# Performance work log

Hardware: AMD Instinct MI355X
Metric: run time of the kernel (lower is better)

## Reference

```python
import jax, jax.numpy as jnp
import numpy as np

B, T, N_EMBD = 4, 2048, 1024
NUM_EXPERTS, TOP_K = 8, 2
N_CITIES = 4
LIN = N_EMBD + 32 + N_EMBD // 4 + N_EMBD // 4 + N_EMBD // 8 + N_EMBD // 8  # 1824


def setup_inputs() -> dict:
    key = jax.random.key(0)
    ks = jax.random.split(key, 12)
    s = 0.02  # init std as in _init_weights
    return {
        "x": jax.random.normal(ks[0], (B, T, N_EMBD), jnp.float32),
        "delta_t_info": jax.random.normal(ks[1], (B, T, N_EMBD // 4), jnp.float32),
        "delta_dis_info": jax.random.normal(ks[2], (B, T, N_EMBD // 4), jnp.float32),
        "delta_rg_info": jax.random.normal(ks[3], (B, T, N_EMBD // 8), jnp.float32),
        "delta_entropy_info": jax.random.normal(ks[4], (B, T, N_EMBD // 8), jnp.float32),
        "city_embeddings": jax.random.normal(ks[5], (N_CITIES, 32), jnp.float32),
        "Wg": jax.random.normal(ks[6], (LIN, NUM_EXPERTS), jnp.float32) * s,
        "bg": jnp.zeros((NUM_EXPERTS,), jnp.float32),
        "W1": jax.random.normal(ks[7], (NUM_EXPERTS, N_EMBD, 4 * N_EMBD), jnp.float32) * s,
        "b1": jnp.zeros((NUM_EXPERTS, 4 * N_EMBD), jnp.float32),
        "W2": jax.random.normal(ks[8], (NUM_EXPERTS, 4 * N_EMBD, N_EMBD), jnp.float32) * s,
        "b2": jnp.zeros((NUM_EXPERTS, N_EMBD), jnp.float32),
        "city_index": 1,
    }


def _moe(x, dt, dd, drg, de, city_embeddings, Wg, bg, W1, b1, W2, b2, city_index):
    b, t, _ = x.shape
    city = jnp.broadcast_to(city_embeddings[city_index], (b, t, 32))
    feats = jnp.concatenate([x, city, dt, dd, drg, de], axis=-1)  # [B,T,LIN]
    logits = jnp.einsum("btl,le->bte", feats, Wg) + bg            # eval mode: no noise
    gate1 = jax.nn.softmax(logits, axis=-1)
    _, topi = jax.lax.top_k(logits, TOP_K)                        # [B,T,k]
    # mask of top-k experts per token; scatter(-inf elsewhere) + softmax
    mask = jax.nn.one_hot(topi, NUM_EXPERTS, dtype=jnp.float32).sum(axis=-2) > 0
    sparse_logits = jnp.where(mask, logits, -jnp.inf)
    gates = jax.nn.softmax(sparse_logits, axis=-1)                # zeros outside top-k
    out = jnp.zeros_like(x)
    for e in range(NUM_EXPERTS):  # fixed small expert set
        h = jax.nn.gelu(jnp.einsum("btc,ch->bth", x, W1[e]) + b1[e], approximate=True)
        y = jnp.einsum("bth,hc->btc", h, W2[e]) + b2[e]
        out = out + gates[..., e:e + 1] * y  # gate is exactly 0 for non-topk tokens
    return out, gate1


def reference(x, delta_t_info, delta_dis_info, delta_rg_info, delta_entropy_info,
              city_embeddings, Wg, bg, W1, b1, W2, b2, city_index):
    return _moe(x, delta_t_info, delta_dis_info, delta_rg_info, delta_entropy_info,
                city_embeddings, Wg, bg, W1, b1, W2, b2, city_index)
```

## Files before the change

### kernel.cpp

```cpp
#include <hip/hip_runtime.h>
#include <hip/hip_bf16.h>
#include <stdint.h>

#define NTOK 8192
#define DEMB 1024
#define HDIM 4096
#define NEXP 8
#define LINF 1824
#define MAXPAD 17280

typedef __attribute__((ext_vector_type(8))) __bf16 bf16x8;
typedef __attribute__((ext_vector_type(4))) __bf16 bf16x4v;
typedef __attribute__((ext_vector_type(4))) float f32x4;

__device__ __forceinline__ void gload_lds16(const void* g, void* l) {
  __builtin_amdgcn_global_load_lds(
      (const __attribute__((address_space(1))) void*)g,
      (__attribute__((address_space(3))) void*)l, 16, 0, 0);
}

__device__ __forceinline__ float dot4(float4 a, float4 b) {
  return a.x*b.x + a.y*b.y + a.z*b.z + a.w*b.w;
}

__global__ void __launch_bounds__(256) k_logits(
    const float* __restrict__ x, const float* __restrict__ dt,
    const float* __restrict__ dd, const float* __restrict__ drg,
    const float* __restrict__ de, const float* __restrict__ city,
    const float* __restrict__ Wg, const float* __restrict__ bg,
    const int* __restrict__ city_index,
    float* __restrict__ gate1, int* __restrict__ top_i, float2* __restrict__ top_g)
{
  __shared__ float WgT[NEXP * LINF];
  const int tid = threadIdx.x;
  const float4* Wg4 = (const float4*)Wg;
  for (int i = tid; i < LINF * NEXP / 4; i += 256) {
    float4 v = Wg4[i];
    int e0 = (i & 1) * 4, f = i >> 1;
    WgT[(e0+0)*LINF + f] = v.x; WgT[(e0+1)*LINF + f] = v.y;
    WgT[(e0+2)*LINF + f] = v.z; WgT[(e0+3)*LINF + f] = v.w;
  }
  __syncthreads();

  const int wave = tid >> 6, lane = tid & 63;
  const int ci = city_index[0];
  const float4* city4 = (const float4*)(city + ci*32);
  const float4 z4 = {0.f, 0.f, 0.f, 0.f};

  #pragma unroll
  for (int k = 0; k < 4; ++k) {
    const int t = blockIdx.x*16 + wave*4 + k;
    const float4* x4 = (const float4*)x + (size_t)t*256;
    float4 xv0 = x4[lane], xv1 = x4[64+lane], xv2 = x4[128+lane], xv3 = x4[192+lane];
    float4 cv = (lane < 8) ? city4[lane] : z4;
    float4 tv = ((const float4*)dt)[(size_t)t*64 + lane];
    float4 dv = ((const float4*)dd)[(size_t)t*64 + lane];
    float4 rv = z4, ev = z4;
    if (lane < 32) {
      rv = ((const float4*)drg)[(size_t)t*32 + lane];
      ev = ((const float4*)de )[(size_t)t*32 + lane];
    }
    float a[8];
    const int l8 = lane & 7, l32 = lane & 31;
    #pragma unroll
    for (int e = 0; e < 8; ++e) {
      const float4* W = (const float4*)(WgT + e*LINF);
      float s = dot4(xv0, W[lane]) + dot4(xv1, W[64+lane])
              + dot4(xv2, W[128+lane]) + dot4(xv3, W[192+lane]);
      s += dot4(cv, W[256 + l8]);
      s += dot4(tv, W[264 + lane]) + dot4(dv, W[328 + lane]);
      s += dot4(rv, W[392 + l32]) + dot4(ev, W[424 + l32]);
      a[e] = s;
    }
    #pragma unroll
    for (int off = 32; off > 0; off >>= 1)
      #pragma unroll
      for (int e = 0; e < 8; ++e) a[e] += __shfl_xor(a[e], off);

    float lg[8];
    #pragma unroll
    for (int e = 0; e < 8; ++e) lg[e] = a[e] + bg[e];
    float mx = lg[0];
    #pragma unroll
    for (int e = 1; e < 8; ++e) mx = fmaxf(mx, lg[e]);
    float ex[8]; float s = 0.f;
    #pragma unroll
    for (int e = 0; e < 8; ++e) { ex[e] = expf(lg[e] - mx); s += ex[e]; }
    int i1 = 0; float l1 = lg[0];
    #pragma unroll
    for (int e = 1; e < 8; ++e) if (lg[e] > l1) { l1 = lg[e]; i1 = e; }
    int i2 = -1; float l2 = -1e30f;
    #pragma unroll
    for (int e = 0; e < 8; ++e) if (e != i1 && lg[e] > l2) { l2 = lg[e]; i2 = e; }
    float e2 = expf(l2 - l1);

    if (lane == 0) {
      float inv = 1.f / s;
      float4 o0 = { ex[0]*inv, ex[1]*inv, ex[2]*inv, ex[3]*inv };
      float4 o1 = { ex[4]*inv, ex[5]*inv, ex[6]*inv, ex[7]*inv };
      float4* gp = (float4*)(gate1 + (size_t)t*8);
      gp[0] = o0; gp[1] = o1;
      top_i[t] = i1 | (i2 << 4);
      float2 g = { 1.f / (1.f + e2), e2 / (1.f + e2) };
      top_g[t] = g;
    }
  }
}

__global__ void __launch_bounds__(256) k_build(
    const int* __restrict__ top_i, const float2* __restrict__ top_g,
    int* __restrict__ counts, int* __restrict__ ex_tok, float* __restrict__ ex_gate,
    int2* __restrict__ ppos)
{
  __shared__ int lcnt[8], lbase[8];
  const int tid = threadIdx.x;
  if (tid < 8) lcnt[tid] = 0;
  __syncthreads();
  const int t = blockIdx.x*256 + tid;
  const int ti = top_i[t];
  const int i1 = ti & 15, i2 = ti >> 4;
  const float2 g = top_g[t];
  int p1 = atomicAdd(&lcnt[i1], 1);
  int p2 = atomicAdd(&lcnt[i2], 1);
  __syncthreads();
  if (tid < 8) lbase[tid] = atomicAdd(&counts[tid], lcnt[tid]);
  __syncthreads();
  int s1 = lbase[i1] + p1; ex_tok[i1*NTOK+s1] = t; ex_gate[i1*NTOK+s1] = g.x;
  int s2 = lbase[i2] + p2; ex_tok[i2*NTOK+s2] = t; ex_gate[i2*NTOK+s2] = g.y;
  int2 pp = { i1 | (s1 << 3), i2 | (s2 << 3) };
  ppos[t] = pp;
}

__global__ void k_finalize(const int* __restrict__ counts, int* __restrict__ seg) {
  if (threadIdx.x == 0 && blockIdx.x == 0) {
    int s = 0;
    for (int e = 0; e < 8; ++e) { seg[e] = s; s += (counts[e] + 127) & ~127; }
    seg[8] = s;
  }
}

__global__ void __launch_bounds__(256) k_conv_x(
    const float4* __restrict__ x, bf16x4v* __restrict__ xb, int n4)
{
  int step = gridDim.x * blockDim.x;
  for (int i = blockIdx.x*blockDim.x + threadIdx.x; i < n4; i += step) {
    float4 v = x[i];
    bf16x4v o;
    o[0] = (__bf16)v.x; o[1] = (__bf16)v.y; o[2] = (__bf16)v.z; o[3] = (__bf16)v.w;
    xb[i] = o;
  }
}

template<int RDIM, int CDIM>
__global__ void __launch_bounds__(256) k_tconv(
    const float* __restrict__ W, __bf16* __restrict__ WT)
{
  const int e  = blockIdx.z;
  const int c0 = blockIdx.x * 64, r0 = blockIdx.y * 64;
  __shared__ float tbuf[64][65];
  const float* src = W  + (size_t)e * RDIM * CDIM;
  __bf16*      dst = WT + (size_t)e * RDIM * CDIM;
  const int tx = threadIdx.x & 63, ty = threadIdx.x >> 6;
  #pragma unroll
  for (int rr = ty; rr < 64; rr += 4)
    tbuf[rr][tx] = src[(size_t)(r0+rr)*CDIM + c0 + tx];
  __syncthreads();
  #pragma unroll
  for (int cc = ty; cc < 64; cc += 4)
    dst[(size_t)(c0+cc)*RDIM + r0 + tx] = (__bf16)tbuf[tx][cc];
}

template<int KDIM, int NDIM, bool G1>
__global__ void __launch_bounds__(256) k_moe_gemm(
    const __bf16* __restrict__ Abase, const __bf16* __restrict__ WT,
    const float* __restrict__ bias,
    const int* __restrict__ seg, const int* __restrict__ counts,
    const int* __restrict__ ex_tok,
    int chunk0, __bf16* __restrict__ dstbuf)
{
  const int nx = gridDim.x, ny = gridDim.y;
  const int nwg = nx * ny;
  int flat = blockIdx.x + nx * blockIdx.y;
  {
    int q = nwg >> 3, r = nwg & 7;
    int xcd = flat & 7, idx = flat >> 3;
    flat = (xcd < r ? xcd * (q + 1) : r * (q + 1) + (xcd - r) * q) + idx;
  }
  int bx, by;
  if (G1) { bx = flat % nx; by = flat / nx; }
  else    { by = flat % ny; bx = flat / ny; }

  const int segtot = seg[8];
  const int row0 = chunk0 + bx * 128;
  if (row0 >= segtot) return;
  int e = 0;
  #pragma unroll
  for (int qq = 1; qq < 8; ++qq) if (row0 >= seg[qq]) e = qq;
  const int cnt  = counts[e];
  const int sege = seg[e];
  const int n0 = by * 128;

  __shared__ __align__(16) char smem[32768];
  __bf16* Alds = (__bf16*)smem;
  __bf16* Blds = (__bf16*)(smem + 16384);

  const int tid = threadIdx.x;
  const int w = tid >> 6, lane = tid & 63;
  const __bf16* Bsrc = WT + (size_t)e * NDIM * KDIM;

  const __bf16* asrc[4]; const __bf16* bsrc[4];
  #pragma unroll
  for (int i = 0; i < 4; ++i) {
    int g = w*256 + i*64 + lane;
    int rr = g >> 3;
    int bi = (g & 7) ^ (rr & 7);
    int prow = row0 + rr;
    int arow;
    if (G1) {
      int lr = prow - sege;
      arow = (lr < cnt) ? ex_tok[e*NTOK + lr] : 0;
    } else {
      arow = prow - chunk0;
    }
    asrc[i] = Abase + (size_t)arow * KDIM + bi*8;
    bsrc[i] = Bsrc  + (size_t)(n0 + rr) * KDIM + bi*8;
  }

  f32x4 acc[4][4] = {};
  const int wrow = (w >> 1) * 64, wcol = (w & 1) * 64;
  const int l15 = lane & 15, l4 = lane >> 4;

  for (int k0 = 0; k0 < KDIM; k0 += 64) {
    #pragma unroll
    for (int i = 0; i < 4; ++i) {
      gload_lds16(asrc[i] + k0, (char*)Alds + (w*256 + i*64)*16);
      gload_lds16(bsrc[i] + k0, (char*)Blds + (w*256 + i*64)*16);
    }
    __syncthreads();
    #pragma unroll
    for (int kk = 0; kk < 2; ++kk) {
      bf16x8 af[4], bfv[4];
      const int kblk = kk*4 + l4;
      #pragma unroll
      for (int m = 0; m < 4; ++m) {
        int rr = wrow + m*16 + l15;
        af[m] = *(const bf16x8*)((const char*)Alds + rr*128 + ((kblk ^ (rr & 7)) * 16));
      }
      #pragma unroll
      for (int n = 0; n < 4; ++n) {
        int cc = wcol + n*16 + l15;
        bfv[n] = *(const bf16x8*)((const char*)Blds + cc*128 + ((kblk ^ (cc & 7)) * 16));
      }
      #pragma unroll
      for (int m = 0; m < 4; ++m)
        #pragma unroll
        for (int n = 0; n < 4; ++n)
          acc[m][n] = __builtin_amdgcn_mfma_f32_16x16x32_bf16(af[m], bfv[n], acc[m][n], 0, 0, 0);
    }
    __syncthreads();
  }

  __bf16* Cl = (__bf16*)smem;
  #pragma unroll
  for (int n = 0; n < 4; ++n) {
    int gcol = n0 + wcol + n*16 + l15;
    float bv = bias[(size_t)e*NDIM + gcol];
    #pragma unroll
    for (int m = 0; m < 4; ++m) {
      #pragma unroll
      for (int r2 = 0; r2 < 4; ++r2) {
        float v = acc[m][n][r2] + bv;
        if (G1) {
          float z = 2.302208f * (v + 0.044715f * v * v * v);
          v = v / (1.f + exp2f(-z));
        }
        Cl[(wrow + m*16 + l4*4 + r2)*128 + wcol + n*16 + l15] = (__bf16)v;
      }
    }
  }
  __syncthreads();
  const int drow0 = G1 ? (row0 - chunk0) : row0;
  #pragma unroll
  for (int it = 0; it < 8; ++it) {
    int idx2 = it*256 + tid;
    int rr = idx2 >> 4, c8 = (idx2 & 15) * 8;
    *(bf16x8*)(dstbuf + (size_t)(drow0 + rr)*NDIM + n0 + c8) =
        *(const bf16x8*)(Cl + rr*128 + c8);
  }
}

__global__ void __launch_bounds__(256) k_combine(
    const __bf16* __restrict__ pbuf, const int2* __restrict__ ppos,
    const float2* __restrict__ top_g, const int* __restrict__ seg,
    float* __restrict__ out)
{
  const int t = blockIdx.x;
  const int tid = threadIdx.x;
  const int2 pp = ppos[t];
  const float2 g = top_g[t];
  const int e1 = pp.x & 7, i1 = pp.x >> 3;
  const int e2 = pp.y & 7, i2 = pp.y >> 3;
  const __bf16* r1 = pbuf + (size_t)(seg[e1] + i1) * DEMB;
  const __bf16* r2 = pbuf + (size_t)(seg[e2] + i2) * DEMB;
  float* orow = out + (size_t)t * DEMB;
  const int c = tid * 4;
  bf16x4v a = *(const bf16x4v*)(r1 + c);
  bf16x4v b = *(const bf16x4v*)(r2 + c);
  float4 o;
  o.x = g.x*(float)a[0] + g.y*(float)b[0];
  o.y = g.x*(float)a[1] + g.y*(float)b[1];
  o.z = g.x*(float)a[2] + g.y*(float)b[2];
  o.w = g.x*(float)a[3] + g.y*(float)b[3];
  *(float4*)(orow + c) = o;
}

extern "C" void kernel_launch(void* const* d_in, const int* in_sizes, int n_in,
                              void* d_out, int out_size, void* d_ws, size_t ws_size,
                              hipStream_t stream)
{
  const float* x   = (const float*)d_in[0];
  const float* dt  = (const float*)d_in[1];
  const float* dd  = (const float*)d_in[2];
  const float* drg = (const float*)d_in[3];
  const float* de  = (const float*)d_in[4];
  const float* city= (const float*)d_in[5];
  const float* Wg  = (const float*)d_in[6];
  const float* bg  = (const float*)d_in[7];
  const float* W1  = (const float*)d_in[8];
  const float* b1  = (const float*)d_in[9];
  const float* W2  = (const float*)d_in[10];
  const float* b2  = (const float*)d_in[11];
  const int* city_index = (const int*)d_in[12];

  float* out   = (float*)d_out;
  float* gate1 = out + (size_t)NTOK * DEMB;

  char* p = (char*)d_ws;
  int*    counts  = (int*)p;      p += 256;
  int*    seg     = (int*)p;      p += 256;
  int*    top_i   = (int*)p;      p += (size_t)NTOK*4;
  float2* top_g   = (float2*)p;   p += (size_t)NTOK*8;
  int2*   ppos    = (int2*)p;     p += (size_t)NTOK*8;
  int*    ex_tok  = (int*)p;      p += (size_t)NTOK*NEXP*4;
  float*  ex_gate = (float*)p;    p += (size_t)NTOK*NEXP*4;
  __bf16* xb      = (__bf16*)p;   p += (size_t)NTOK*DEMB*2;
  __bf16* W1T     = (__bf16*)p;   p += (size_t)NEXP*DEMB*HDIM*2;
  __bf16* W2T     = (__bf16*)p;   p += (size_t)NEXP*DEMB*HDIM*2;
  __bf16* pbuf    = (__bf16*)p;   p += (size_t)MAXPAD*DEMB*2;
  __bf16* hbuf    = (__bf16*)p;

  size_t fixed = (size_t)(p - (char*)d_ws);
  int CH = MAXPAD;
  while (CH > 0 && fixed + (size_t)CH * HDIM * 2 > ws_size) CH -= 128;
  if (CH <= 0) return;
  int nch = (MAXPAD + CH - 1) / CH;

  (void)hipMemsetAsync(counts, 0, 64, stream);

  k_conv_x<<<2048, 256, 0, stream>>>((const float4*)x, (bf16x4v*)xb, NTOK*DEMB/4);
  k_tconv<DEMB, HDIM><<<dim3(HDIM/64, DEMB/64, NEXP), 256, 0, stream>>>(W1, W1T);
  k_tconv<HDIM, DEMB><<<dim3(DEMB/64, HDIM/64, NEXP), 256, 0, stream>>>(W2, W2T);

  k_logits<<<NTOK/16, 256, 0, stream>>>(x, dt, dd, drg, de, city, Wg, bg,
                                        city_index, gate1, top_i, top_g);
  k_build<<<NTOK/256, 256, 0, stream>>>(top_i, top_g, counts, ex_tok, ex_gate, ppos);
  k_finalize<<<1, 64, 0, stream>>>(counts, seg);

  for (int c = 0; c < nch; ++c) {
    k_moe_gemm<DEMB, HDIM, true><<<dim3(CH/128, HDIM/128), 256, 0, stream>>>(
        xb, W1T, b1, seg, counts, ex_tok, c*CH, hbuf);
    k_moe_gemm<HDIM, DEMB, false><<<dim3(CH/128, DEMB/128), 256, 0, stream>>>(
        hbuf, W2T, b2, seg, counts, ex_tok, c*CH, pbuf);
  }
  k_combine<<<NTOK, 256, 0, stream>>>(pbuf, ppos, top_g, seg, out);
}
```

Before: 639.8 us.

## Triple-buffer MoE GEMM with 128x256 tiles and 512-thread workgroups

Widens the grouped expert GEMM tile to 128x256 with 8 waves per workgroup and replaces the single-buffer load/sync loop with a three-stage LDS ring. Global-to-LDS loads for the stage two steps ahead are issued before the current MFMAs, with explicit vmcnt waits and raw barriers. It also precomputes the swizzled LDS offsets and bias values and raises wave priority around the MFMA block. The aim is to hide global memory latency and reuse each A tile across more output columns, at the cost of 144KB of LDS per block, lower occupancy, and fragile hand-written wait counts.

```diff
diff --git a/kernel.cpp b/kernel.cpp
--- a/kernel.cpp
+++ b/kernel.cpp
@@ -171,13 +171,16 @@
 }
 
 template<int KDIM, int NDIM, bool G1>
-__global__ void __launch_bounds__(256) k_moe_gemm(
+__global__ void __launch_bounds__(512, 2) k_moe_gemm(
     const __bf16* __restrict__ Abase, const __bf16* __restrict__ WT,
     const float* __restrict__ bias,
     const int* __restrict__ seg, const int* __restrict__ counts,
     const int* __restrict__ ex_tok,
     int chunk0, __bf16* __restrict__ dstbuf)
 {
+  constexpr int NT = KDIM / 64;
+  constexpr int BUFB = 49152;
+
   const int nx = gridDim.x, ny = gridDim.y;
   const int nwg = nx * ny;
   int flat = blockIdx.x + nx * blockIdx.y;
@@ -198,83 +201,121 @@
   for (int qq = 1; qq < 8; ++qq) if (row0 >= seg[qq]) e = qq;
   const int cnt  = counts[e];
   const int sege = seg[e];
-  const int n0 = by * 128;
-
-  __shared__ __align__(16) char smem[32768];
-  __bf16* Alds = (__bf16*)smem;
-  __bf16* Blds = (__bf16*)(smem + 16384);
+  const int n0 = by * 256;
+
+  __shared__ __align__(16) char smem[3 * BUFB];
 
   const int tid = threadIdx.x;
-  const int w = tid >> 6, lane = tid & 63;
+  const int wid = tid >> 6, lane = tid & 63;
+  const int wm = wid >> 2, wn = wid & 3;
+  const int l15 = lane & 15, l4 = lane >> 4;
   const __bf16* Bsrc = WT + (size_t)e * NDIM * KDIM;
 
-  const __bf16* asrc[4]; const __bf16* bsrc[4];
-  #pragma unroll
-  for (int i = 0; i < 4; ++i) {
-    int g = w*256 + i*64 + lane;
+  const __bf16* asrc[2]; const __bf16* bsrc[4];
+  #pragma unroll
+  for (int i = 0; i < 2; ++i) {
+    int g = i*512 + tid;
     int rr = g >> 3;
-    int bi = (g & 7) ^ (rr & 7);
-    int prow = row0 + rr;
+    int kb = (g & 7) ^ (rr & 7);
     int arow;
     if (G1) {
-      int lr = prow - sege;
+      int lr = row0 + rr - sege;
       arow = (lr < cnt) ? ex_tok[e*NTOK + lr] : 0;
     } else {
-      arow = prow - chunk0;
-    }
-    asrc[i] = Abase + (size_t)arow * KDIM + bi*8;
-    bsrc[i] = Bsrc  + (size_t)(n0 + rr) * KDIM + bi*8;
-  }
+      arow = row0 + rr - chunk0;
+    }
+    asrc[i] = Abase + (size_t)arow * KDIM + kb*8;
+  }
+  #pragma unroll
+  for (int i = 0; i < 4; ++i) {
+    int g = i*512 + tid;
+    int rr = g >> 3;
+    int kb = (g & 7) ^ (rr & 7);
+    bsrc[i] = Bsrc + (size_t)(n0 + rr) * KDIM + kb*8;
+  }
+
+  int aoff[2][4], boff[2][4];
+  #pragma unroll
+  for (int kk = 0; kk < 2; ++kk) {
+    const int kblk = kk*4 + l4;
+    const int xo = (kblk ^ (l15 & 7)) * 16;
+    #pragma unroll
+    for (int m = 0; m < 4; ++m)
+      aoff[kk][m] = (wm*64 + m*16 + l15)*128 + xo;
+    #pragma unroll
+    for (int n = 0; n < 4; ++n)
+      boff[kk][n] = 16384 + (wn*64 + n*16 + l15)*128 + xo;
+  }
+
+  float bv[4];
+  #pragma unroll
+  for (int n = 0; n < 4; ++n)
+    bv[n] = bias[(size_t)e*NDIM + n0 + wn*64 + n*16 + l15];
+
+  auto STAGE = [&](int t, int b) {
+    char* base = smem + b*BUFB;
+    #pragma unroll
+    for (int i = 0; i < 2; ++i)
+      gload_lds16(asrc[i] + t*64, base + (i*512 + tid)*16);
+    #pragma unroll
+    for (int i = 0; i < 4; ++i)
+      gload_lds16(bsrc[i] + t*64, base + 16384 + (i*512 + tid)*16);
+  };
 
   f32x4 acc[4][4] = {};
-  const int wrow = (w >> 1) * 64, wcol = (w & 1) * 64;
-  const int l15 = lane & 15, l4 = lane >> 4;
-
-  for (int k0 = 0; k0 < KDIM; k0 += 64) {
-    #pragma unroll
-    for (int i = 0; i < 4; ++i) {
-      gload_lds16(asrc[i] + k0, (char*)Alds + (w*256 + i*64)*16);
-      gload_lds16(bsrc[i] + k0, (char*)Blds + (w*256 + i*64)*16);
-    }
-    __syncthreads();
+
+  STAGE(0, 0);
+  STAGE(1, 1);
+  asm volatile("s_waitcnt vmcnt(6)" ::: "memory");
+  __builtin_amdgcn_s_barrier();
+  __builtin_amdgcn_sched_barrier(0);
+
+  int cur = 0;
+  for (int t = 0; t < NT; ++t) {
+    const char* cb = smem + cur*BUFB;
+    if (t + 2 < NT) {
+      int b2 = cur + 2; if (b2 >= 3) b2 -= 3;
+      __builtin_amdgcn_sched_barrier(0);
+      STAGE(t + 2, b2);
+      __builtin_amdgcn_sched_barrier(0);
+    }
     #pragma unroll
     for (int kk = 0; kk < 2; ++kk) {
       bf16x8 af[4], bfv[4];
-      const int kblk = kk*4 + l4;
       #pragma unroll
-      for (int m = 0; m < 4; ++m) {
-        int rr = wrow + m*16 + l15;
-        af[m] = *(const bf16x8*)((const char*)Alds + rr*128 + ((kblk ^ (rr & 7)) * 16));
-      }
+      for (int m = 0; m < 4; ++m) af[m]  = *(const bf16x8*)(cb + aoff[kk][m]);
       #pragma unroll
-      for (int n = 0; n < 4; ++n) {
-        int cc = wcol + n*16 + l15;
-        bfv[n] = *(const bf16x8*)((const char*)Blds + cc*128 + ((kblk ^ (cc & 7)) * 16));
-      }
+      for (int n = 0; n < 4; ++n) bfv[n] = *(const bf16x8*)(cb + boff[kk][n]);
+      __builtin_amdgcn_s_setprio(1);
       #pragma unroll
       for (int m = 0; m < 4; ++m)
         #pragma unroll
         for (int n = 0; n < 4; ++n)
           acc[m][n] = __builtin_amdgcn_mfma_f32_16x16x32_bf16(af[m], bfv[n], acc[m][n], 0, 0, 0);
-    }
-    __syncthreads();
+      __builtin_amdgcn_s_setprio(0);
+    }
+    __builtin_amdgcn_sched_barrier(0);
+    asm volatile("s_waitcnt lgkmcnt(0)" ::: "memory");
+    if (t + 2 < NT) asm volatile("s_waitcnt vmcnt(6)" ::: "memory");
+    else            asm volatile("s_waitcnt vmcnt(0)" ::: "memory");
+    __builtin_amdgcn_s_barrier();
+    __builtin_amdgcn_sched_barrier(0);
+    cur = (cur == 2) ? 0 : cur + 1;
   }
 
   __bf16* Cl = (__bf16*)smem;
   #pragma unroll
   for (int n = 0; n < 4; ++n) {
-    int gcol = n0 + wcol + n*16 + l15;
-    float bv = bias[(size_t)e*NDIM + gcol];
     #pragma unroll
     for (int m = 0; m < 4; ++m) {
       #pragma unroll
       for (int r2 = 0; r2 < 4; ++r2) {
-        float v = acc[m][n][r2] + bv;
+        float v = acc[m][n][r2] + bv[n];
         if (G1) {
           float z = 2.302208f * (v + 0.044715f * v * v * v);
           v = v / (1.f + exp2f(-z));
         }
-        Cl[(wrow + m*16 + l4*4 + r2)*128 + wcol + n*16 + l15] = (__bf16)v;
+        Cl[(wm*64 + m*16 + l4*4 + r2)*256 + wn*64 + n*16 + l15] = (__bf16)v;
       }
     }
   }
@@ -282,10 +323,10 @@
   const int drow0 = G1 ? (row0 - chunk0) : row0;
   #pragma unroll
   for (int it = 0; it < 8; ++it) {
-    int idx2 = it*256 + tid;
-    int rr = idx2 >> 4, c8 = (idx2 & 15) * 8;
+    int idx2 = it*512 + tid;
+    int rr = idx2 >> 5, c8 = (idx2 & 31) * 8;
     *(bf16x8*)(dstbuf + (size_t)(drow0 + rr)*NDIM + n0 + c8) =
-        *(const bf16x8*)(Cl + rr*128 + c8);
+        *(const bf16x8*)(Cl + rr*256 + c8);
   }
 }
 
@@ -351,7 +392,7 @@
 
   size_t fixed = (size_t)(p - (char*)d_ws);
   int CH = MAXPAD;
-  while (CH > 0 && fixed + (size_t)CH * HDIM * 2 > ws_size) CH -= 128;
+  while (CH > 0 && fixed + (size_t)CH * HDIM * 2 > ws_size) CH -= 256;
   if (CH <= 0) return;
   int nch = (MAXPAD + CH - 1) / CH;
 
@@ -367,9 +408,9 @@
   k_finalize<<<1, 64, 0, stream>>>(counts, seg);
 
   for (int c = 0; c < nch; ++c) {
-    k_moe_gemm<DEMB, HDIM, true><<<dim3(CH/128, HDIM/128), 256, 0, stream>>>(
+    k_moe_gemm<DEMB, HDIM, true><<<dim3(CH/128, HDIM/256), 512, 0, stream>>>(
         xb, W1T, b1, seg, counts, ex_tok, c*CH, hbuf);
-    k_moe_gemm<HDIM, DEMB, false><<<dim3(CH/128, DEMB/128), 256, 0, stream>>>(
+    k_moe_gemm<HDIM, DEMB, false><<<dim3(CH/128, DEMB/256), 512, 0, stream>>>(
         hbuf, W2T, b2, seg, counts, ex_tok, c*CH, pbuf);
   }
   k_combine<<<NTOK, 256, 0, stream>>>(pbuf, ppos, top_g, seg, out);
```

Result: faster. 589.2 us (-7.9%).
